# Kernel tuning notes

Measured on AMD Instinct MI355X. Metric: run time of the kernel, lower is better.

The kernel has to match this reference:

```python
import jax, jax.numpy as jnp
import numpy as np

B, L, D, H = 32, 256, 2048, 8
DH = D // H  # 256; code requires L == S == DH


def setup_inputs() -> dict:
    key = jax.random.key(0)
    ks = jax.random.split(key, 12)
    s = 1.0 / np.sqrt(D)
    return {
        "queries": jax.random.normal(ks[0], (B, L, D), jnp.float32),
        "keys": jax.random.normal(ks[1], (B, L, D), jnp.float32),
        "values": jax.random.normal(ks[2], (B, L, D), jnp.float32),
        "Wq": jax.random.normal(ks[3], (D, D), jnp.float32) * s,
        "bq": jax.random.normal(ks[4], (D,), jnp.float32) * s,
        "Wk": jax.random.normal(ks[5], (D, D), jnp.float32) * s,
        "bk": jax.random.normal(ks[6], (D,), jnp.float32) * s,
        "Wv": jax.random.normal(ks[7], (D, D), jnp.float32) * s,
        "bv": jax.random.normal(ks[8], (D,), jnp.float32) * s,
        "Wo": jax.random.normal(ks[9], (D, D), jnp.float32) * s,
        "bo": jax.random.normal(ks[10], (D,), jnp.float32) * s,
        "temperature": jnp.ones((H, 1, 1), jnp.float32),
    }


def reference(queries, keys, values, Wq, bq, Wk, bk, Wv, bv, Wo, bo, temperature):
    b, l, d = queries.shape
    # projections (Linear: x @ W^T + b)
    q = (jnp.einsum('bld,ed->ble', queries, Wq) + bq).reshape(b, l, H, DH).transpose(0, 2, 1, 3)   # [B,H,L,dh]
    k = (jnp.einsum('bsd,ed->bse', keys, Wk) + bk).reshape(b, l, H, DH).transpose(0, 2, 1, 3)      # [B,H,S,dh]
    v = (jnp.einsum('bsd,ed->bse', values, Wv) + bv).reshape(b, l, H, DH).transpose(0, 2, 3, 1)    # [B,H,dh,S]
    # FFT cross-correlation over the head dim (as in the source)
    qf = jnp.fft.rfft(q, axis=-1)
    kf = jnp.fft.rfft(k, axis=-1)
    corr = jnp.fft.irfft(qf * jnp.conj(kf), n=DH, axis=-1)   # [B,H,L,dh]
    corr = jax.nn.softmax(corr / temperature, axis=-1)
    # dropout is identity in eval mode
    # time-delay aggregation: [B,H,dh,S] @ [B,H,dh,L] (S == dh) -> [B,H,dh,L]
    out = jnp.matmul(v, jnp.swapaxes(corr, -1, -2))
    out = out.transpose(0, 3, 1, 2).reshape(b, l, d)          # [B,L,D]
    out = jnp.einsum('bld,ed->ble', out, Wo) + bo
    return out
```

## Files before the change

kernel.cpp:

```cpp
#include <hip/hip_runtime.h>
#include <stdint.h>

typedef float  f32x4 __attribute__((ext_vector_type(4)));
typedef short  s16x8 __attribute__((ext_vector_type(8)));
typedef _Float16 h16x8 __attribute__((ext_vector_type(8)));
typedef unsigned short u16x4 __attribute__((ext_vector_type(4)));

#define DEV __device__ __forceinline__

DEV unsigned short f2bf(float f) {
  union { float f; unsigned int u; } v; v.f = f;
  unsigned int u = v.u;
  return (unsigned short)((u + 0x7fffu + ((u >> 16) & 1u)) >> 16);
}

typedef const __attribute__((address_space(1))) void* as1cvp;
typedef __attribute__((address_space(3))) void* as3vp;
DEV void gload16(const void* g, void* l) {
  __builtin_amdgcn_global_load_lds((as1cvp)g, (as3vp)l, 16, 0, 0);
}


__global__ __launch_bounds__(256) void pack_f16(const float* __restrict__ in,
                                                unsigned short* __restrict__ out, long total8)
{
  for (long t = (long)blockIdx.x * 256 + threadIdx.x; t < total8;
       t += (long)gridDim.x * 256) {
    const float* src = in + t * 8;
    f32x4 x0 = *(const f32x4*)src;
    f32x4 x1 = *(const f32x4*)(src + 4);
    s16x8 h8;
    #pragma unroll
    for (int e = 0; e < 4; ++e) {
      h8[e]     = (short)__builtin_bit_cast(unsigned short, (_Float16)x0[e]);
      h8[e + 4] = (short)__builtin_bit_cast(unsigned short, (_Float16)x1[e]);
    }
    *(s16x8*)(out + t * 8) = h8;
  }
}

__global__ __launch_bounds__(256) void pack_bf16(const float* __restrict__ in,
                                                 unsigned short* __restrict__ out, long total8)
{
  for (long t = (long)blockIdx.x * 256 + threadIdx.x; t < total8;
       t += (long)gridDim.x * 256) {
    const float* src = in + t * 8;
    f32x4 x0 = *(const f32x4*)src;
    f32x4 x1 = *(const f32x4*)(src + 4);
    s16x8 h8;
    #pragma unroll
    for (int e = 0; e < 4; ++e) {
      h8[e]     = (short)f2bf(x0[e]);
      h8[e + 4] = (short)f2bf(x1[e]);
    }
    *(s16x8*)(out + t * 8) = h8;
  }
}

template<int DT>
DEV f32x4 mfma16(s16x8 a, s16x8 b, f32x4 c) {
  if constexpr (DT == 0)
    return __builtin_amdgcn_mfma_f32_16x16x32_bf16(a, b, c, 0, 0, 0);
  else
    return __builtin_amdgcn_mfma_f32_16x16x32_f16(
        __builtin_bit_cast(h16x8, a), __builtin_bit_cast(h16x8, b), c, 0, 0, 0);
}

template<int DT, int OM>
__global__ __launch_bounds__(512, 2)
void gemm8p(const unsigned short* __restrict__ Ap, const unsigned short* __restrict__ Bp,
            const float* __restrict__ bias, void* __restrict__ Cp)
{
  constexpr int LD  = 2048;
  constexpr int LDC = 2048;
  constexpr int NT  = 32;
  constexpr int NI  = NT / 2;

  __shared__ __align__(16) unsigned short lds[65536];

  const int tid  = threadIdx.x;
  const int lane = tid & 63;
  const int wid  = tid >> 6;
  const int wm   = wid >> 2;
  const int wn   = wid & 3;
  const int fr   = lane & 15;
  const int ko   = (lane >> 4) * 8;

  const int bx = blockIdx.x;
  const int m0 = (((bx & 7) << 2) + (bx >> 3)) * 256;
  const int n0 = blockIdx.y * 256;

  const int sr  = tid >> 3;
  const int scc = (((tid & 7) ^ (((tid >> 5) & 1) << 2)) << 3);

  auto sA = [&](int d, int u, int col) {
    const unsigned short* s0 = Ap + (long)(m0 + u * 64 + sr) * LD + col + scc;
    const int lb = d * 32768 + u * 4096 + (wid << 9);
    gload16(s0, lds + lb);
    gload16(s0 + 128 * LD, lds + lb + 8192);
  };
  auto sB = [&](int d, int h, int col) {
    const unsigned short* s0 = Bp + (long)(n0 + h * 128 + sr) * LD + col + scc;
    const int lb = d * 32768 + 16384 + h * 8192 + (wid << 9);
    gload16(s0, lds + lb);
    gload16(s0 + 64 * LD, lds + lb + 4096);
  };

  f32x4 acc[8][4];
  #pragma unroll
  for (int i = 0; i < 8; ++i)
    #pragma unroll
    for (int j = 0; j < 4; ++j)
      acc[i][j] = (f32x4)(0.0f);

  s16x8 afr[2][2], bfr[4][2];

#define LOADB(d)                                                              \
  _Pragma("unroll") for (int ni = 0; ni < 4; ++ni)                            \
    _Pragma("unroll") for (int kk = 0; kk < 2; ++kk) {                        \
      const int nr = wn * 64 + ni * 16 + fr;                                  \
      int u = (d) * 32768 + 16384 + (nr >> 7) * 8192 + (nr & 127) * 64        \
              + kk * 32 + ko;                                                 \
      u ^= ((u >> 8) & 1) << 5;                                               \
      bfr[ni][kk] = *(const s16x8*)&lds[u];                                   \
    }

#define PHASE(d, q, DOB, STAGE, VM)                                           \
  {                                                                           \
    if (DOB) { LOADB(d) }                                                     \
    _Pragma("unroll") for (int ai = 0; ai < 2; ++ai)                          \
      _Pragma("unroll") for (int kk = 0; kk < 2; ++kk) {                      \
        int u = (d) * 32768 + wm * 8192 + ((2 * (q) + ai) * 16 + fr) * 64     \
                + kk * 32 + ko;                                               \
        u ^= ((u >> 8) & 1) << 5;                                             \
        afr[ai][kk] = *(const s16x8*)&lds[u];                                 \
      }                                                                       \
    STAGE;                                                                    \
    __builtin_amdgcn_s_barrier();                                             \
    asm volatile("s_waitcnt lgkmcnt(0)" ::: "memory");                        \
    __builtin_amdgcn_sched_barrier(0);                                        \
    __builtin_amdgcn_s_setprio(1);                                            \
    _Pragma("unroll") for (int ai = 0; ai < 2; ++ai)                          \
      _Pragma("unroll") for (int ni = 0; ni < 4; ++ni)                        \
        _Pragma("unroll") for (int kk = 0; kk < 2; ++kk)                      \
          acc[2 * (q) + ai][ni] =                                             \
              mfma16<DT>(afr[ai][kk], bfr[ni][kk], acc[2 * (q) + ai][ni]);    \
    __builtin_amdgcn_s_setprio(0);                                            \
    if (VM) { asm volatile("s_waitcnt vmcnt(6)" ::: "memory"); }              \
    __builtin_amdgcn_s_barrier();                                             \
  }

  sB(0, 0, 0); sB(0, 1, 0);
  sA(0, 0, 0); sA(0, 1, 0);
  sB(1, 0, 64); sB(1, 1, 64);
  sA(1, 0, 64);
  asm volatile("s_waitcnt vmcnt(6)" ::: "memory");
  __builtin_amdgcn_s_barrier();

  for (int i = 0; i < NI; ++i) {
    const int a1c = (2 * i + 1) << 6;
    const int c0  = ((2 * i + 2 < NT) ? 2 * i + 2 : NT - 1) << 6;
    const int c1  = ((2 * i + 3 < NT) ? 2 * i + 3 : NT - 1) << 6;
    PHASE(0, 0, true,  sA(1, 1, a1c), false)
    PHASE(0, 1, false, sB(0, 0, c0), false)
    PHASE(0, 2, false, sB(0, 1, c0), false)
    PHASE(0, 3, false, sA(0, 0, c0), true)
    PHASE(1, 0, true,  sA(0, 1, c0), false)
    PHASE(1, 1, false, sB(1, 0, c1), false)
    PHASE(1, 2, false, sB(1, 1, c1), false)
    PHASE(1, 3, false, sA(1, 0, c1), true)
  }
#undef PHASE
#undef LOADB

  const int rg = (lane >> 4) * 4;
  #pragma unroll
  for (int ni = 0; ni < 4; ++ni) {
    const int gn = n0 + wn * 64 + ni * 16 + fr;
    const float bvl = bias[gn];
    #pragma unroll
    for (int mi = 0; mi < 8; ++mi) {
      const int gmB = m0 + wm * 128 + mi * 16 + rg;
      f32x4 v = acc[mi][ni];
      if (OM == 0) {
        float* Cf = (float*)Cp;
        #pragma unroll
        for (int r = 0; r < 4; ++r)
          Cf[(long)(gmB + r) * LDC + gn] = v[r] + bvl;
      } else {
        const int b = gmB >> 8, s = gmB & 255, h = gn >> 8, ii = gn & 255;
        u16x4 o;
        #pragma unroll
        for (int r = 0; r < 4; ++r) o[r] = f2bf(v[r] + bvl);
        *(u16x4*)&((unsigned short*)Cp)[((long)((b * 8 + h) * 256 + ii) << 8) + s] = o;
      }
    }
  }
}

template<int MODE, int OM, bool BATCHED>
__global__ __launch_bounds__(256)
void fgemm(const unsigned short* __restrict__ A, const unsigned short* __restrict__ B,
           const float* __restrict__ bias, void* __restrict__ C,
           int lda, int ldb, int ldc, int KT)
{
  __shared__ __align__(16) unsigned short lA[2 * 128 * 32];
  __shared__ __align__(16) unsigned short lB[2 * 128 * 32];

  const int tid  = threadIdx.x;
  const int lane = tid & 63;
  const int wid  = tid >> 6;
  const int wr   = wid >> 1;
  const int wc   = wid & 1;

  const int z  = BATCHED ? blockIdx.z : 0;
  const int m0 = blockIdx.y * 128;
  const int n0 = blockIdx.x * 128;

  long aBase = (long)m0 * lda;
  long bBase = (long)n0 * ldb;
  if (BATCHED) {
    aBase += (long)z * 256 * lda;
    bBase += (long)z * 256 * ldb;
  }

  const int ar0 = tid >> 2, ac0 = (tid & 3) * 8;
  const int ar1 = ar0 + 64, ac1 = ac0;

  const unsigned short* pa0 = A + aBase + (long)ar0 * lda + ac0;
  const unsigned short* pa1 = A + aBase + (long)ar1 * lda + ac1;
  const unsigned short* pb0 = B + bBase + (long)ar0 * ldb + ac0;
  const unsigned short* pb1 = B + bBase + (long)ar1 * ldb + ac1;

  constexpr int SUBOFF = (MODE == 0) ? 2048 : 32;
  constexpr int KSTEP  = (MODE == 0) ? 32 : 64;

  f32x4 acc[4][4];
  #pragma unroll
  for (int i = 0; i < 4; ++i)
    #pragma unroll
    for (int j = 0; j < 4; ++j)
      acc[i][j] = (f32x4)(0.0f);

  const int fr   = lane & 15;
  const int krow = (lane >> 4) * 8;

  for (int kt = 0; kt < KT; kt += KSTEP) {
    gload16(pa0 + kt,          lA + tid * 8);
    gload16(pa1 + kt,          lA + (tid + 256) * 8);
    gload16(pa0 + kt + SUBOFF, lA + 4096 + tid * 8);
    gload16(pa1 + kt + SUBOFF, lA + 4096 + (tid + 256) * 8);
    gload16(pb0 + kt,          lB + tid * 8);
    gload16(pb1 + kt,          lB + (tid + 256) * 8);
    gload16(pb0 + kt + SUBOFF, lB + 4096 + tid * 8);
    gload16(pb1 + kt + SUBOFF, lB + 4096 + (tid + 256) * 8);
    __syncthreads();

    s16x8 a0[4], a1[4], b0[4], b1[4];
    #pragma unroll
    for (int i = 0; i < 4; ++i) {
      const int r = (wr * 64 + i * 16 + fr) * 32 + krow;
      a0[i] = *(const s16x8*)&lA[r];
      a1[i] = *(const s16x8*)&lA[4096 + r];
    }
    #pragma unroll
    for (int j = 0; j < 4; ++j) {
      const int r = (wc * 64 + j * 16 + fr) * 32 + krow;
      b0[j] = *(const s16x8*)&lB[r];
      b1[j] = *(const s16x8*)&lB[4096 + r];
    }

    #pragma unroll
    for (int i = 0; i < 4; ++i)
      #pragma unroll
      for (int j = 0; j < 4; ++j) {
        if (MODE == 0) {
          acc[i][j] = __builtin_amdgcn_mfma_f32_16x16x32_bf16(a1[i], b0[j], acc[i][j], 0, 0, 0);
          acc[i][j] = __builtin_amdgcn_mfma_f32_16x16x32_bf16(a0[i], b1[j], acc[i][j], 0, 0, 0);
          acc[i][j] = __builtin_amdgcn_mfma_f32_16x16x32_bf16(a0[i], b0[j], acc[i][j], 0, 0, 0);
        } else {
          acc[i][j] = __builtin_amdgcn_mfma_f32_16x16x32_bf16(a0[i], b0[j], acc[i][j], 0, 0, 0);
          acc[i][j] = __builtin_amdgcn_mfma_f32_16x16x32_bf16(a1[i], b1[j], acc[i][j], 0, 0, 0);
        }
      }

    __syncthreads();
  }

  const int rg = (lane >> 4) * 4;
  #pragma unroll
  for (int j = 0; j < 4; ++j) {
    const int gn = n0 + wc * 64 + j * 16 + fr;
    const float bvl = bias ? bias[gn] : 0.0f;
    #pragma unroll
    for (int i = 0; i < 4; ++i) {
      const int gmB = m0 + wr * 64 + i * 16 + rg;
      f32x4 v = acc[i][j];
      if (OM == 0) {
        float* Cf = (float*)C;
        #pragma unroll
        for (int r = 0; r < 4; ++r)
          Cf[(long)(gmB + r) * ldc + gn] = v[r] + bvl;
      } else if (OM == 2) {
        long cb = 0;
        if (BATCHED) cb = (long)(z >> 3) * 256 * ldc + (long)(z & 7) * 256;
        unsigned short* Ch = (unsigned short*)C;
        #pragma unroll
        for (int r = 0; r < 4; ++r)
          Ch[cb + (long)(gmB + r) * ldc + gn] = f2bf(v[r] + bvl);
      } else {
        const int b = gmB >> 8, s = gmB & 255, h = gn >> 8, ii = gn & 255;
        u16x4 o;
        #pragma unroll
        for (int r = 0; r < 4; ++r) o[r] = f2bf(v[r] + bvl);
        *(u16x4*)&((unsigned short*)C)[((long)((b * 8 + h) * 256 + ii) << 8) + s] = o;
      }
    }
  }
}

__global__ __launch_bounds__(256)
void corr_softmax(const float* __restrict__ qp, const float* __restrict__ kp0,
                  const float* __restrict__ kp1, const float* __restrict__ temp,
                  unsigned short* __restrict__ w)
{
  __shared__ float qs[4][520];
  __shared__ float ks[4][264];
  const int tid  = threadIdx.x;
  const int lane = tid & 63;
  const int wid  = tid >> 6;
  const int row  = blockIdx.x * 4 + wid;
  const int b = row >> 11;
  const int h = (row >> 8) & 7;
  const int l = row & 255;
  const long qbase = ((long)(b * 256 + l) << 11) + h * 256;
  const float* kb  = (b < 16) ? kp0 : kp1;
  const long kbase = ((long)((b & 15) * 256 + l) << 11) + h * 256;

  {
    f32x4 qv = *(const f32x4*)(qp + qbase + 4 * lane);
    f32x4 kv = *(const f32x4*)(kb + kbase + 4 * lane);
    *(f32x4*)&qs[wid][4 * lane]       = qv;
    *(f32x4*)&qs[wid][256 + 4 * lane] = qv;
    *(f32x4*)&ks[wid][4 * lane]       = kv;
  }
  __syncthreads();

  float c0 = 0.f, c1 = 0.f, c2 = 0.f, c3 = 0.f;
  const int d = 4 * lane;
  const float* Q  = &qs[wid][0];
  const float* Kv = &ks[wid][0];
  f32x4 qa = *(const f32x4*)(Q + d);
  #pragma unroll 4
  for (int u0 = 0; u0 < 256; u0 += 4) {
    f32x4 k4 = *(const f32x4*)(Kv + u0);
    f32x4 qb = *(const f32x4*)(Q + u0 + d + 4);
    c0 += k4[0]*qa[0] + k4[1]*qa[1] + k4[2]*qa[2] + k4[3]*qa[3];
    c1 += k4[0]*qa[1] + k4[1]*qa[2] + k4[2]*qa[3] + k4[3]*qb[0];
    c2 += k4[0]*qa[2] + k4[1]*qa[3] + k4[2]*qb[0] + k4[3]*qb[1];
    c3 += k4[0]*qa[3] + k4[1]*qb[0] + k4[2]*qb[1] + k4[3]*qb[2];
    qa = qb;
  }

  const float invT = 1.0f / temp[h];
  float mx = fmaxf(fmaxf(c0, c1), fmaxf(c2, c3));
  #pragma unroll
  for (int off = 32; off >= 1; off >>= 1) mx = fmaxf(mx, __shfl_xor(mx, off, 64));
  const float e0 = __expf((c0 - mx) * invT);
  const float e1 = __expf((c1 - mx) * invT);
  const float e2 = __expf((c2 - mx) * invT);
  const float e3 = __expf((c3 - mx) * invT);
  float sm = e0 + e1 + e2 + e3;
  #pragma unroll
  for (int off = 32; off >= 1; off >>= 1) sm += __shfl_xor(sm, off, 64);
  const float rs = 1.0f / sm;
  u16x4 o;
  o[0] = f2bf(e0 * rs); o[1] = f2bf(e1 * rs); o[2] = f2bf(e2 * rs); o[3] = f2bf(e3 * rs);
  *(u16x4*)(w + (long)row * 256 + d) = o;
}


extern "C" void kernel_launch(void* const* d_in, const int* in_sizes, int n_in,
                              void* d_out, int out_size, void* d_ws, size_t ws_size,
                              hipStream_t stream) {
  (void)in_sizes; (void)n_in; (void)out_size; (void)ws_size;
  const float* queries = (const float*)d_in[0];
  const float* keys    = (const float*)d_in[1];
  const float* values  = (const float*)d_in[2];
  const float* Wq = (const float*)d_in[3];
  const float* bq = (const float*)d_in[4];
  const float* Wk = (const float*)d_in[5];
  const float* bk = (const float*)d_in[6];
  const float* Wv = (const float*)d_in[7];
  const float* bv = (const float*)d_in[8];
  const float* Wo = (const float*)d_in[9];
  const float* bo = (const float*)d_in[10];
  const float* temp = (const float*)d_in[11];

  char* ws = (char*)d_ws;
  auto MB = [](size_t m) { return m << 20; };
  unsigned short* extA = (unsigned short*)ws;
  unsigned short* wgt  = (unsigned short*)ws;
  float*          qproj= (float*)(ws + MB(32));
  unsigned short* vT   = (unsigned short*)(ws + MB(32));
  unsigned short* out2 = (unsigned short*)(ws + MB(64));
  float*          kproj= (float*)(ws + MB(96));
  unsigned short* Wob  = (unsigned short*)(ws + MB(96));
  unsigned short* Vb   = (unsigned short*)(ws + MB(160));
  unsigned short* extW = (unsigned short*)d_out;

  dim3 blk(256);
  dim3 gBig(32, 8);

  pack_f16<<<2048, blk, 0, stream>>>(queries, extA, (long)8192 * 2048 / 8);
  pack_f16<<<2048, blk, 0, stream>>>(Wq, extW, (long)2048 * 2048 / 8);
  gemm8p<1, 0><<<gBig, 512, 0, stream>>>(extA, extW, bq, qproj);
  pack_f16<<<2048, blk, 0, stream>>>(keys, extA, (long)8192 * 2048 / 8);
  pack_f16<<<2048, blk, 0, stream>>>(Wk, extW, (long)2048 * 2048 / 8);
  gemm8p<1, 0><<<gBig, 512, 0, stream>>>(extA, extW, bk, kproj);
  corr_softmax<<<dim3(16384), blk, 0, stream>>>(qproj, kproj,
                                                kproj + (long)16 * 256 * 2048, temp, wgt);
  pack_bf16<<<2048, blk, 0, stream>>>(values, Vb, (long)8192 * 2048 / 8);
  pack_bf16<<<2048, blk, 0, stream>>>(Wv, extW, (long)2048 * 2048 / 8);
  gemm8p<0, 1><<<gBig, 512, 0, stream>>>(Vb, extW, bv, vT);
  fgemm<1, 2, true><<<dim3(2, 2, 256), blk, 0, stream>>>(wgt, vT, nullptr, out2,
                                                         256, 256, 2048, 256);
  pack_bf16<<<2048, blk, 0, stream>>>(Wo, Wob, (long)2048 * 2048 / 8);
  gemm8p<0, 0><<<gBig, 512, 0, stream>>>(out2, Wob, bo, (float*)d_out);
}
```

Baseline: 526.3 us.

## Store Q/K projections as fp16 and compute correlation with packed fdot2

The Q and K projection GEMMs now write fp16 outputs instead of fp32, which halves the intermediate storage and the traffic that corr_softmax reads. corr_softmax keeps a shifted copy of q in shared memory so that odd offsets can be computed with v_dot2 on aligned half2 pairs. The workspace layout is reshuffled to fit the smaller buffers. In exchange, the circular correlation is accumulated from fp16-rounded q and k, which costs some precision.

Result: faster. 462.0 us (-12.2%).

```diff
diff --git a/kernel.cpp b/kernel.cpp
--- a/kernel.cpp
+++ b/kernel.cpp
@@ -4,7 +4,10 @@
 typedef float  f32x4 __attribute__((ext_vector_type(4)));
 typedef short  s16x8 __attribute__((ext_vector_type(8)));
 typedef _Float16 h16x8 __attribute__((ext_vector_type(8)));
+typedef _Float16 h16x2 __attribute__((ext_vector_type(2)));
 typedef unsigned short u16x4 __attribute__((ext_vector_type(4)));
+typedef unsigned int u32x2 __attribute__((ext_vector_type(2)));
+typedef unsigned int u32x4 __attribute__((ext_vector_type(4)));
 
 #define DEV __device__ __forceinline__
 
@@ -18,6 +21,11 @@
 typedef __attribute__((address_space(3))) void* as3vp;
 DEV void gload16(const void* g, void* l) {
   __builtin_amdgcn_global_load_lds((as1cvp)g, (as3vp)l, 16, 0, 0);
+}
+
+DEV float fdot2u(unsigned int a, unsigned int b, float c) {
+  return __builtin_amdgcn_fdot2(__builtin_bit_cast(h16x2, a),
+                                __builtin_bit_cast(h16x2, b), c, false);
 }
 
 
@@ -187,6 +195,12 @@
         #pragma unroll
         for (int r = 0; r < 4; ++r)
           Cf[(long)(gmB + r) * LDC + gn] = v[r] + bvl;
+      } else if (OM == 2) {
+        unsigned short* Ch = (unsigned short*)Cp;
+        #pragma unroll
+        for (int r = 0; r < 4; ++r)
+          Ch[(long)(gmB + r) * LDC + gn] =
+              __builtin_bit_cast(unsigned short, (_Float16)(v[r] + bvl));
       } else {
         const int b = gmB >> 8, s = gmB & 255, h = gn >> 8, ii = gn & 255;
         u16x4 o;
@@ -320,12 +334,13 @@
 }
 
 __global__ __launch_bounds__(256)
-void corr_softmax(const float* __restrict__ qp, const float* __restrict__ kp0,
-                  const float* __restrict__ kp1, const float* __restrict__ temp,
-                  unsigned short* __restrict__ w)
+void corr_softmax(const unsigned short* __restrict__ qp,
+                  const unsigned short* __restrict__ kp,
+                  const float* __restrict__ temp, unsigned short* __restrict__ w)
 {
-  __shared__ float qs[4][520];
-  __shared__ float ks[4][264];
+  __shared__ __align__(16) unsigned short qs[4][520];
+  __shared__ __align__(16) unsigned short q2[4][520];
+  __shared__ __align__(16) unsigned short ks[4][264];
   const int tid  = threadIdx.x;
   const int lane = tid & 63;
   const int wid  = tid >> 6;
@@ -333,33 +348,56 @@
   const int b = row >> 11;
   const int h = (row >> 8) & 7;
   const int l = row & 255;
-  const long qbase = ((long)(b * 256 + l) << 11) + h * 256;
-  const float* kb  = (b < 16) ? kp0 : kp1;
-  const long kbase = ((long)((b & 15) * 256 + l) << 11) + h * 256;
+  const long base = ((long)(b * 256 + l) << 11) + h * 256;
 
   {
-    f32x4 qv = *(const f32x4*)(qp + qbase + 4 * lane);
-    f32x4 kv = *(const f32x4*)(kb + kbase + 4 * lane);
-    *(f32x4*)&qs[wid][4 * lane]       = qv;
-    *(f32x4*)&qs[wid][256 + 4 * lane] = qv;
-    *(f32x4*)&ks[wid][4 * lane]       = kv;
+    u16x4 qv = *(const u16x4*)(qp + base + 4 * lane);
+    u16x4 kv = *(const u16x4*)(kp + base + 4 * lane);
+    const int nxt = __shfl((int)(unsigned int)(unsigned short)qv[0],
+                           (lane + 1) & 63, 64);
+    u16x4 qsv;
+    qsv[0] = qv[1]; qsv[1] = qv[2]; qsv[2] = qv[3];
+    qsv[3] = (unsigned short)(unsigned int)nxt;
+    *(u16x4*)&qs[wid][4 * lane]       = qv;
+    *(u16x4*)&qs[wid][256 + 4 * lane] = qv;
+    *(u16x4*)&q2[wid][4 * lane]       = qsv;
+    *(u16x4*)&q2[wid][256 + 4 * lane] = qsv;
+    *(u16x4*)&ks[wid][4 * lane]       = kv;
   }
   __syncthreads();
 
+  const unsigned short* Q  = &qs[wid][0];
+  const unsigned short* Qs = &q2[wid][0];
+  const unsigned short* K  = &ks[wid][0];
+  const int e = 2 * lane;
+
+  u32x2 A  = *(const u32x2*)&Q[2 * e];
+  u32x2 B  = *(const u32x2*)&Q[2 * (e + 2)];
+  u32x2 C  = *(const u32x2*)&Q[2 * (e + 4)];
+  u32x2 A2 = *(const u32x2*)&Qs[2 * e];
+  u32x2 B2 = *(const u32x2*)&Qs[2 * (e + 2)];
+  u32x2 C2 = *(const u32x2*)&Qs[2 * (e + 4)];
+
   float c0 = 0.f, c1 = 0.f, c2 = 0.f, c3 = 0.f;
-  const int d = 4 * lane;
-  const float* Q  = &qs[wid][0];
-  const float* Kv = &ks[wid][0];
-  f32x4 qa = *(const f32x4*)(Q + d);
-  #pragma unroll 4
-  for (int u0 = 0; u0 < 256; u0 += 4) {
-    f32x4 k4 = *(const f32x4*)(Kv + u0);
-    f32x4 qb = *(const f32x4*)(Q + u0 + d + 4);
-    c0 += k4[0]*qa[0] + k4[1]*qa[1] + k4[2]*qa[2] + k4[3]*qa[3];
-    c1 += k4[0]*qa[1] + k4[1]*qa[2] + k4[2]*qa[3] + k4[3]*qb[0];
-    c2 += k4[0]*qa[2] + k4[1]*qa[3] + k4[2]*qb[0] + k4[3]*qb[1];
-    c3 += k4[0]*qa[3] + k4[1]*qb[0] + k4[2]*qb[1] + k4[3]*qb[2];
-    qa = qb;
+
+  #pragma unroll 2
+  for (int t = 0; t < 32; ++t) {
+    u32x4 Kw = *(const u32x4*)&K[8 * t];
+    const unsigned int p0 = A[0],  p1 = A[1],  p2 = B[0],  p3 = B[1],  p4 = C[0];
+    const unsigned int s0 = A2[0], s1 = A2[1], s2 = B2[0], s3 = B2[1], s4 = C2[0];
+    c0 = fdot2u(Kw[0], p0, c0); c2 = fdot2u(Kw[0], p1, c2);
+    c1 = fdot2u(Kw[0], s0, c1); c3 = fdot2u(Kw[0], s1, c3);
+    c0 = fdot2u(Kw[1], p1, c0); c2 = fdot2u(Kw[1], p2, c2);
+    c1 = fdot2u(Kw[1], s1, c1); c3 = fdot2u(Kw[1], s2, c3);
+    c0 = fdot2u(Kw[2], p2, c0); c2 = fdot2u(Kw[2], p3, c2);
+    c1 = fdot2u(Kw[2], s2, c1); c3 = fdot2u(Kw[2], s3, c3);
+    c0 = fdot2u(Kw[3], p3, c0); c2 = fdot2u(Kw[3], p4, c2);
+    c1 = fdot2u(Kw[3], s3, c1); c3 = fdot2u(Kw[3], s4, c3);
+    A = C;  A2 = C2;
+    B  = *(const u32x2*)&Q[2 * (4 * t + e + 6)];
+    C  = *(const u32x2*)&Q[2 * (4 * t + e + 8)];
+    B2 = *(const u32x2*)&Qs[2 * (4 * t + e + 6)];
+    C2 = *(const u32x2*)&Qs[2 * (4 * t + e + 8)];
   }
 
   const float invT = 1.0f / temp[h];
@@ -376,7 +414,7 @@
   const float rs = 1.0f / sm;
   u16x4 o;
   o[0] = f2bf(e0 * rs); o[1] = f2bf(e1 * rs); o[2] = f2bf(e2 * rs); o[3] = f2bf(e3 * rs);
-  *(u16x4*)(w + (long)row * 256 + d) = o;
+  *(u16x4*)(w + (long)row * 256 + 4 * lane) = o;
 }
 
 
@@ -400,13 +438,13 @@
   char* ws = (char*)d_ws;
   auto MB = [](size_t m) { return m << 20; };
   unsigned short* extA = (unsigned short*)ws;
-  unsigned short* wgt  = (unsigned short*)ws;
-  float*          qproj= (float*)(ws + MB(32));
+  unsigned short* Vb   = (unsigned short*)ws;
+  unsigned short* qproj= (unsigned short*)(ws + MB(32));
   unsigned short* vT   = (unsigned short*)(ws + MB(32));
+  unsigned short* kproj= (unsigned short*)(ws + MB(64));
   unsigned short* out2 = (unsigned short*)(ws + MB(64));
-  float*          kproj= (float*)(ws + MB(96));
-  unsigned short* Wob  = (unsigned short*)(ws + MB(96));
-  unsigned short* Vb   = (unsigned short*)(ws + MB(160));
+  unsigned short* wgt  = (unsigned short*)(ws + MB(96));
+  unsigned short* Wob  = (unsigned short*)(ws + MB(128));
   unsigned short* extW = (unsigned short*)d_out;
 
   dim3 blk(256);
@@ -414,12 +452,11 @@
 
   pack_f16<<<2048, blk, 0, stream>>>(queries, extA, (long)8192 * 2048 / 8);
   pack_f16<<<2048, blk, 0, stream>>>(Wq, extW, (long)2048 * 2048 / 8);
-  gemm8p<1, 0><<<gBig, 512, 0, stream>>>(extA, extW, bq, qproj);
+  gemm8p<1, 2><<<gBig, 512, 0, stream>>>(extA, extW, bq, qproj);
   pack_f16<<<2048, blk, 0, stream>>>(keys, extA, (long)8192 * 2048 / 8);
   pack_f16<<<2048, blk, 0, stream>>>(Wk, extW, (long)2048 * 2048 / 8);
-  gemm8p<1, 0><<<gBig, 512, 0, stream>>>(extA, extW, bk, kproj);
-  corr_softmax<<<dim3(16384), blk, 0, stream>>>(qproj, kproj,
-                                                kproj + (long)16 * 256 * 2048, temp, wgt);
+  gemm8p<1, 2><<<gBig, 512, 0, stream>>>(extA, extW, bk, kproj);
+  corr_softmax<<<dim3(16384), blk, 0, stream>>>(qproj, kproj, temp, wgt);
   pack_bf16<<<2048, blk, 0, stream>>>(values, Vb, (long)8192 * 2048 / 8);
   pack_bf16<<<2048, blk, 0, stream>>>(Wv, extW, (long)2048 * 2048 / 8);
   gemm8p<0, 1><<<gBig, 512, 0, stream>>>(Vb, extW, bv, vT);
```
